# Kernel tuning notes

Measured on AMD Instinct MI355X. Metric: run time of the kernel, lower is better.

## Reference

```python
import jax, jax.numpy as jnp
import numpy as np

EPS = 1e-5
DEPTH = 4       # hash tree depth -> 16 buckets, 15 internal nodes
NBUCKETS = 16


def _bn_relu(x, g, b):
    # training-mode BatchNorm2d over (N,H,W) followed by ReLU
    m = x.mean((0, 2, 3), keepdims=True)
    v = x.var((0, 2, 3), keepdims=True)
    y = (x - m) * jax.lax.rsqrt(v + EPS)
    return jax.nn.relu(y * g[None, :, None, None] + b[None, :, None, None])


def _maddness_encode(sub, split_dims, thresholds):
    # sub: [R, Cb, L] subvectors; split_dims: [Cb, DEPTH] int; thresholds: [Cb, 15]
    R, Cb, _ = sub.shape
    carange = jnp.arange(Cb)[None, :]
    bucket = jnp.zeros((R, Cb), jnp.int32)
    for t in range(DEPTH):
        vals = jnp.take_along_axis(sub, split_dims[None, :, t][..., None], axis=2)[..., 0]  # [R,Cb]
        node = (2 ** t - 1) + bucket                     # node index at this tree level
        thr = thresholds[carange, node]                  # [R,Cb]
        bucket = 2 * bucket + (vals > thr).astype(jnp.int32)
    return bucket                                        # [R,Cb] in [0,16)


def _maddness_conv(x, split_dims, thresholds, lut, ksize, stride, pad):
    # hash-tree encode im2col patches per codebook, then LUT gather-and-sum
    N, C, H, W = x.shape
    patches = jax.lax.conv_general_dilated_patches(
        x, (ksize, ksize), (stride, stride), [(pad, pad), (pad, pad)])  # [N, C*k*k, Ho, Wo], channel-major
    _, Fdim, Ho, Wo = patches.shape
    Cb = split_dims.shape[0]
    sub = patches.transpose(0, 2, 3, 1).reshape(N * Ho * Wo, Cb, Fdim // Cb)
    codes = _maddness_encode(sub, split_dims, thresholds)
    onehot = jax.nn.one_hot(codes, NBUCKETS, dtype=lut.dtype)          # [R,Cb,16]
    out = jnp.einsum('rck,cko->ro', onehot, lut)                       # LUT gather-sum as GEMM
    return out.reshape(N, Ho, Wo, lut.shape[-1]).transpose(0, 3, 1, 2)


def setup_inputs() -> dict:
    key = jax.random.key(0)
    ks = jax.random.split(key, 16)
    P_in, P_out = 128, 256
    Cb1, Cb2, CbS = P_in, P_out, P_in // 4
    inp = {
        'x': jax.random.normal(ks[0], (32, P_in, 56, 56), jnp.float32),
        'bn1_g': jnp.ones((P_in,), jnp.float32),
        'bn1_b': jnp.zeros((P_in,), jnp.float32),
        'bn2_g': jnp.ones((P_out,), jnp.float32),
        'bn2_b': jnp.zeros((P_out,), jnp.float32),
        'thr1': jax.random.normal(ks[1], (Cb1, 15), jnp.float32),
        'lut1': 0.02 * jax.random.normal(ks[2], (Cb1, 16, P_out), jnp.float32),
        'thr2': jax.random.normal(ks[3], (Cb2, 15), jnp.float32),
        'lut2': 0.02 * jax.random.normal(ks[4], (Cb2, 16, P_out), jnp.float32),
        'thr_s': jax.random.normal(ks[5], (CbS, 15), jnp.float32),
        'lut_s': 0.02 * jax.random.normal(ks[6], (CbS, 16, P_out), jnp.float32),
        'fc1_w': 0.05 * jax.random.normal(ks[7], (P_out // 16, P_out), jnp.float32),
        'fc1_b': jnp.zeros((P_out // 16,), jnp.float32),
        'fc2_w': 0.05 * jax.random.normal(ks[8], (P_out, P_out // 16), jnp.float32),
        'fc2_b': jnp.zeros((P_out,), jnp.float32),
        'sd1': jax.random.randint(ks[9], (Cb1, DEPTH), 0, 9, jnp.int32),
        'sd2': jax.random.randint(ks[10], (Cb2, DEPTH), 0, 9, jnp.int32),
        'sd_s': jax.random.randint(ks[11], (CbS, DEPTH), 0, 4, jnp.int32),
    }
    return inp


def reference(x, bn1_g, bn1_b, bn2_g, bn2_b, thr1, lut1, thr2, lut2,
              thr_s, lut_s, fc1_w, fc1_b, fc2_w, fc2_b, sd1, sd2, sd_s):
    out = _bn_relu(x, bn1_g, bn1_b)
    shortcut = _maddness_conv(out, sd_s, thr_s, lut_s, 1, 2, 0)        # 1x1 stride-2 shortcut
    out = _maddness_conv(out, sd1, thr1, lut1, 3, 2, 1)                # conv1
    out = _maddness_conv(_bn_relu(out, bn2_g, bn2_b), sd2, thr2, lut2, 3, 1, 1)  # conv2
    # SE gate: global avg pool -> fc1 -> relu -> fc2 -> sigmoid
    w = out.mean((2, 3), keepdims=True)                                # [N,P,1,1]
    w = jax.nn.relu(jnp.einsum('nchw,oc->nohw', w, fc1_w) + fc1_b[None, :, None, None])
    w = jax.nn.sigmoid(jnp.einsum('nchw,oc->nohw', w, fc2_w) + fc2_b[None, :, None, None])
    return out * w + shortcut
```

## Files before the change

kernel.cpp:

```cpp
#include <hip/hip_runtime.h>
#include <hip/hip_bf16.h>
#include <math.h>

typedef unsigned char u8;
typedef unsigned int  u32;

#define N_    32
#define C1    128
#define H1    56
#define W1    56
#define HW1   (H1*W1)
#define CHW1  (C1*HW1)
#define C2    256
#define HO    28
#define WO    28
#define OHW   (HO*WO)
#define R_    (N_*OHW)

#define OFF_BN1S   ((size_t)0)
#define OFF_BN1Q   ((size_t)1024)
#define OFF_BN2S   ((size_t)2048)
#define OFF_BN2Q   ((size_t)4096)
#define OFF_POOL   ((size_t)6144)
#define OFF_SCALE1 ((size_t)38912)
#define OFF_SHIFT1 ((size_t)39936)
#define OFF_SCALE2 ((size_t)40960)
#define OFF_SHIFT2 ((size_t)43008)
#define OFF_GATE   ((size_t)45056)
#define OFF_CODE1  ((size_t)77824)
#define OFF_CODES  ((size_t)3289088)
#define OFF_CODE2  ((size_t)4091904)
#define OFF_OUT1   ((size_t)10514432)
#define OFF_SC     ((size_t)61894656)
#define OFF_OUT2   ((size_t)87584768)

__global__ __launch_bounds__(256) void k_bn1_stats(const float* __restrict__ x,
                                                   double* __restrict__ s1, double* __restrict__ q1) {
  __shared__ double rs[256], rq[256];
  int b = blockIdx.x; int c = b >> 3, chunk = b & 7;
  int tid = threadIdx.x;
  double s = 0.0, q = 0.0;
  for (int nn = chunk*4; nn < chunk*4 + 4; ++nn) {
    const float* p = x + (size_t)nn*CHW1 + (size_t)c*HW1;
    for (int i = tid; i < HW1; i += 256) { double v = (double)p[i]; s += v; q += v*v; }
  }
  rs[tid] = s; rq[tid] = q; __syncthreads();
  for (int st = 128; st > 0; st >>= 1) {
    if (tid < st) { rs[tid] += rs[tid+st]; rq[tid] += rq[tid+st]; }
    __syncthreads();
  }
  if (tid == 0) { atomicAdd(&s1[c], rs[0]); atomicAdd(&q1[c], rq[0]); }
}

__global__ __launch_bounds__(256) void k_fin(const double* __restrict__ s, const double* __restrict__ q,
                                             const float* __restrict__ g, const float* __restrict__ b,
                                             double* __restrict__ scale, double* __restrict__ shift,
                                             int nc, double cnt) {
  int c = blockIdx.x*blockDim.x + threadIdx.x;
  if (c >= nc) return;
  double m   = s[c] / cnt;
  double var = q[c] / cnt - m*m;
  double istd = 1.0 / sqrt(var + 1e-5);
  double sc = istd * (double)g[c];
  scale[c] = sc;
  shift[c] = (double)b[c] - m*sc;
}

__global__ __launch_bounds__(256) void k_enc1(const float* __restrict__ x,
                                              const int* __restrict__ sd1, const float* __restrict__ thr1,
                                              const int* __restrict__ sds, const float* __restrict__ thrs,
                                              const double* __restrict__ scale1, const double* __restrict__ shift1,
                                              u8* __restrict__ code1, u8* __restrict__ codes) {
  __shared__ double lsc[C1], lsh[C1];
  __shared__ float lthr[32*15];
  __shared__ u8 lsd[32][4];
  int tid = threadIdx.x;
  int y = blockIdx.y;
  int cbase = (y < 4) ? y*32 : 0;
  if (tid < C1) { lsc[tid] = scale1[tid]; lsh[tid] = shift1[tid]; }
  if (y < 4) {
    for (int i = tid; i < 32*15; i += 256) lthr[i] = thr1[cbase*15 + i];
    if (tid < 32) for (int j = 0; j < 4; ++j) lsd[tid][j] = (u8)sd1[(cbase+tid)*4 + j];
  } else {
    for (int i = tid; i < 32*15; i += 256) lthr[i] = thrs[i];
    if (tid < 32) for (int j = 0; j < 4; ++j) lsd[tid][j] = (u8)sds[tid*4 + j];
  }
  __syncthreads();
  int r = blockIdx.x*256 + tid;
  int n = r / OHW; int rem = r % OHW; int ho = rem / WO; int wo = rem % WO;
  const float* xn = x + (size_t)n*CHW1;
  if (y < 4) {
    for (int ci = 0; ci < 32; ++ci) {
      int c = cbase + ci;
      double sc = lsc[c], sh = lsh[c];
      int code = 0;
      #pragma unroll
      for (int t = 0; t < 4; ++t) {
        int sd = lsd[ci][t];
        int kh = sd / 3, kw = sd - kh*3;
        int ih = 2*ho + kh - 1, iw = 2*wo + kw - 1;
        double thr = (double)lthr[ci*15 + ((1<<t)-1) + code];
        int bit;
        if ((unsigned)ih < (unsigned)H1 && (unsigned)iw < (unsigned)W1) {
          double z = fma((double)xn[c*HW1 + ih*W1 + iw], sc, sh);
          z = z > 0.0 ? z : 0.0;
          bit = (z > thr) ? 1 : 0;
        } else {
          bit = (0.0 > thr) ? 1 : 0;
        }
        code = code + code + bit;
      }
      code1[(size_t)r*C1 + c] = (u8)code;
    }
  } else {
    int base = (2*ho)*W1 + 2*wo;
    for (int ci = 0; ci < 32; ++ci) {
      int code = 0;
      #pragma unroll
      for (int t = 0; t < 4; ++t) {
        int sd = lsd[ci][t];
        int ch = ci*4 + sd;
        double thr = (double)lthr[ci*15 + ((1<<t)-1) + code];
        double z = fma((double)xn[ch*HW1 + base], lsc[ch], lsh[ch]);
        z = z > 0.0 ? z : 0.0;
        int bit = (z > thr) ? 1 : 0;
        code = code + code + bit;
      }
      codes[(size_t)r*32 + ci] = (u8)code;
    }
  }
}

__global__ __launch_bounds__(256) void k_gather1(const u8* __restrict__ code1, const u8* __restrict__ codes,
                                                 const float* __restrict__ lut1, const float* __restrict__ luts,
                                                 double* __restrict__ out1, float* __restrict__ sc) {
  int l = threadIdx.x & 63;
  int r = blockIdx.x*4 + (threadIdx.x >> 6);
  const u32* cp = (const u32*)(code1 + (size_t)r*C1);
  const float4* L = (const float4*)lut1;
  double a0=0,a1=0,a2=0,a3=0;
  #pragma unroll 4
  for (int w = 0; w < 32; ++w) {
    u32 cv = cp[w];
    #pragma unroll
    for (int j = 0; j < 4; ++j) {
      int c = w*4 + j;
      int code = (cv >> (8*j)) & 15;
      float4 v = L[((c*16 + code) << 6) + l];
      a0 += (double)v.x; a1 += (double)v.y; a2 += (double)v.z; a3 += (double)v.w;
    }
  }
  float b0=0,b1=0,b2=0,b3=0;
  const u32* cps = (const u32*)(codes + (size_t)r*32);
  const float4* Ls = (const float4*)luts;
  #pragma unroll
  for (int w = 0; w < 8; ++w) {
    u32 cv = cps[w];
    #pragma unroll
    for (int j = 0; j < 4; ++j) {
      int c = w*4 + j;
      int code = (cv >> (8*j)) & 15;
      float4 v = Ls[((c*16 + code) << 6) + l];
      b0 += v.x; b1 += v.y; b2 += v.z; b3 += v.w;
    }
  }
  size_t o = (size_t)r*C2 + l*4;
  double2 d0; d0.x=a0; d0.y=a1;
  double2 d1; d1.x=a2; d1.y=a3;
  *(double2*)(out1 + o)     = d0;
  *(double2*)(out1 + o + 2) = d1;
  float4 bb; bb.x=b0; bb.y=b1; bb.z=b2; bb.w=b3;
  *(float4*)(sc + o) = bb;
}

__global__ __launch_bounds__(256) void k_bn2_stats(const double* __restrict__ out1,
                                                   double* __restrict__ s2, double* __restrict__ q2) {
  int o = threadIdx.x;
  int r0 = blockIdx.x * 128;
  double s = 0.0, q = 0.0;
  for (int j = 0; j < 128; ++j) {
    double v = out1[(size_t)(r0 + j)*C2 + o];
    s += v; q += v*v;
  }
  atomicAdd(&s2[o], s); atomicAdd(&q2[o], q);
}

__global__ __launch_bounds__(256) void k_enc2(const double* __restrict__ out1,
                                              const int* __restrict__ sd2, const float* __restrict__ thr2,
                                              const double* __restrict__ scale2, const double* __restrict__ shift2,
                                              u8* __restrict__ code2) {
  __shared__ float lthr[C2*15];
  __shared__ u8 lsd[C2][4];
  __shared__ double lsc[C2], lsh[C2];
  int tid = threadIdx.x;
  for (int i = tid; i < C2*15; i += 256) lthr[i] = thr2[i];
  for (int j = 0; j < 4; ++j) lsd[tid][j] = (u8)sd2[tid*4 + j];
  lsc[tid] = scale2[tid]; lsh[tid] = shift2[tid];
  __syncthreads();
  int c = tid;
  double scv = lsc[c], shv = lsh[c];
  int r0 = blockIdx.x*8;
  for (int rr = 0; rr < 8; ++rr) {
    int r = r0 + rr;
    int n = r / OHW; int rem = r % OHW; int ho = rem / WO; int wo = rem % WO;
    const double* on = out1 + (size_t)n*OHW*C2;
    int code = 0;
    #pragma unroll
    for (int t = 0; t < 4; ++t) {
      int sd = lsd[c][t];
      int kh = sd / 3, kw = sd - kh*3;
      int h = ho + kh - 1, w = wo + kw - 1;
      double thr = (double)lthr[c*15 + ((1<<t)-1) + code];
      int bit;
      if ((unsigned)h < (unsigned)HO && (unsigned)w < (unsigned)WO) {
        double z = fma(on[(size_t)(h*WO + w)*C2 + c], scv, shv);
        z = z > 0.0 ? z : 0.0;
        bit = (z > thr) ? 1 : 0;
      } else {
        bit = (0.0 > thr) ? 1 : 0;
      }
      code = code + code + bit;
    }
    code2[(size_t)r*C2 + c] = (u8)code;
  }
}

__global__ __launch_bounds__(256) void k_gather2(const u8* __restrict__ code2,
                                                 const float* __restrict__ lut2, float* __restrict__ out2) {
  int l = threadIdx.x & 63;
  int r = blockIdx.x*4 + (threadIdx.x >> 6);
  const u32* cp = (const u32*)(code2 + (size_t)r*C2);
  const float4* L = (const float4*)lut2;
  float a0=0,a1=0,a2=0,a3=0;
  #pragma unroll 4
  for (int w = 0; w < 64; ++w) {
    u32 cv = cp[w];
    #pragma unroll
    for (int j = 0; j < 4; ++j) {
      int c = w*4 + j;
      int code = (cv >> (8*j)) & 15;
      float4 v = L[((c*16 + code) << 6) + l];
      a0 += v.x; a1 += v.y; a2 += v.z; a3 += v.w;
    }
  }
  float4 res; res.x=a0; res.y=a1; res.z=a2; res.w=a3;
  *(float4*)(out2 + (size_t)r*C2 + l*4) = res;
}

__global__ __launch_bounds__(256) void k_pool(const float* __restrict__ out2, float* __restrict__ pool) {
  int n = blockIdx.x, seg = blockIdx.y, o = threadIdx.x;
  float s = 0.0f;
  int p0 = seg*112;
  for (int p = p0; p < p0 + 112; ++p) s += out2[(size_t)(n*OHW + p)*C2 + o];
  atomicAdd(&pool[n*C2 + o], s);
}

__global__ __launch_bounds__(256) void k_se(const float* __restrict__ pool,
                                            const float* __restrict__ w1, const float* __restrict__ b1f,
                                            const float* __restrict__ w2, const float* __restrict__ b2f,
                                            float* __restrict__ gate) {
  __shared__ float lp[C2];
  __shared__ float lh[16];
  int n = blockIdx.x, tid = threadIdx.x;
  lp[tid] = pool[n*C2 + tid] * (1.0f/(float)OHW);
  __syncthreads();
  if (tid < 16) {
    float s = b1f[tid];
    for (int c = 0; c < C2; ++c) s += lp[c]*w1[tid*C2 + c];
    lh[tid] = s > 0.0f ? s : 0.0f;
  }
  __syncthreads();
  float s = b2f[tid];
  #pragma unroll
  for (int i = 0; i < 16; ++i) s += lh[i]*w2[tid*16 + i];
  gate[n*C2 + tid] = 1.0f/(1.0f + expf(-s));
}

__global__ __launch_bounds__(256) void k_final(const float* __restrict__ out2, const float* __restrict__ scv,
                                               const float* __restrict__ gate, float* __restrict__ outp) {
  int idx = blockIdx.x*256 + threadIdx.x;
  int w = idx % WO; int t1 = idx / WO; int h = t1 % HO; int t2 = t1 / HO;
  int o = t2 & 255; int n = t2 >> 8;
  size_t rc = (size_t)(n*OHW + h*WO + w)*C2 + o;
  outp[idx] = out2[rc]*gate[n*C2 + o] + scv[rc];
}

extern "C" void kernel_launch(void* const* d_in, const int* in_sizes, int n_in,
                              void* d_out, int out_size, void* d_ws, size_t ws_size,
                              hipStream_t stream) {
  const float* x     = (const float*)d_in[0];
  const float* bn1_g = (const float*)d_in[1];
  const float* bn1_b = (const float*)d_in[2];
  const float* bn2_g = (const float*)d_in[3];
  const float* bn2_b = (const float*)d_in[4];
  const float* thr1  = (const float*)d_in[5];
  const float* lut1  = (const float*)d_in[6];
  const float* thr2  = (const float*)d_in[7];
  const float* lut2  = (const float*)d_in[8];
  const float* thr_s = (const float*)d_in[9];
  const float* lut_s = (const float*)d_in[10];
  const float* fc1_w = (const float*)d_in[11];
  const float* fc1_b = (const float*)d_in[12];
  const float* fc2_w = (const float*)d_in[13];
  const float* fc2_b = (const float*)d_in[14];
  const int*   sd1   = (const int*)d_in[15];
  const int*   sd2   = (const int*)d_in[16];
  const int*   sd_s  = (const int*)d_in[17];

  char* ws = (char*)d_ws;
  double* bn1s  = (double*)(ws + OFF_BN1S);
  double* bn1q  = (double*)(ws + OFF_BN1Q);
  double* bn2s  = (double*)(ws + OFF_BN2S);
  double* bn2q  = (double*)(ws + OFF_BN2Q);
  float*  pool  = (float*)(ws + OFF_POOL);
  double* scale1= (double*)(ws + OFF_SCALE1);
  double* shift1= (double*)(ws + OFF_SHIFT1);
  double* scale2= (double*)(ws + OFF_SCALE2);
  double* shift2= (double*)(ws + OFF_SHIFT2);
  float*  gate  = (float*)(ws + OFF_GATE);
  u8*     code1 = (u8*)(ws + OFF_CODE1);
  u8*     codes = (u8*)(ws + OFF_CODES);
  u8*     code2 = (u8*)(ws + OFF_CODE2);
  double* out1  = (double*)(ws + OFF_OUT1);
  float*  scb   = (float*)(ws + OFF_SC);
  float*  out2  = (float*)(ws + OFF_OUT2);
  float*  outp  = (float*)d_out;

  hipMemsetAsync(ws, 0, 38912, stream);

  k_bn1_stats<<<1024, 256, 0, stream>>>(x, bn1s, bn1q);
  k_fin<<<1, 128, 0, stream>>>(bn1s, bn1q, bn1_g, bn1_b, scale1, shift1, C1, (double)(N_*HW1));
  k_enc1<<<dim3(98, 5), 256, 0, stream>>>(x, sd1, thr1, sd_s, thr_s, scale1, shift1, code1, codes);
  k_gather1<<<R_/4, 256, 0, stream>>>(code1, codes, lut1, lut_s, out1, scb);
  k_bn2_stats<<<196, 256, 0, stream>>>(out1, bn2s, bn2q);
  k_fin<<<1, 256, 0, stream>>>(bn2s, bn2q, bn2_g, bn2_b, scale2, shift2, C2, (double)R_);
  k_enc2<<<R_/8, 256, 0, stream>>>(out1, sd2, thr2, scale2, shift2, code2);
  k_gather2<<<R_/4, 256, 0, stream>>>(code2, lut2, out2);
  k_pool<<<dim3(N_, 7), 256, 0, stream>>>(out2, pool);
  k_se<<<N_, 256, 0, stream>>>(pool, fc1_w, fc1_b, fc2_w, fc2_b, gate);
  k_final<<<(int)((size_t)N_*C2*OHW/256), 256, 0, stream>>>(out2, scb, gate, outp);
}
```

Measured before the change: 695.4 us.

## Pack codes to nibbles, use bf16 LUTs, fuse stats/pool, tile final transpose

```diff
diff --git a/kernel.cpp b/kernel.cpp
--- a/kernel.cpp
+++ b/kernel.cpp
@@ -4,6 +4,7 @@
 
 typedef unsigned char u8;
 typedef unsigned int  u32;
+typedef unsigned long long u64;
 
 #define N_    32
 #define C1    128
@@ -27,12 +28,30 @@
 #define OFF_SCALE2 ((size_t)40960)
 #define OFF_SHIFT2 ((size_t)43008)
 #define OFF_GATE   ((size_t)45056)
-#define OFF_CODE1  ((size_t)77824)
-#define OFF_CODES  ((size_t)3289088)
-#define OFF_CODE2  ((size_t)4091904)
-#define OFF_OUT1   ((size_t)10514432)
-#define OFF_SC     ((size_t)61894656)
-#define OFF_OUT2   ((size_t)87584768)
+#define OFF_C1P    ((size_t)77824)
+#define OFF_CS     ((size_t)1683456)
+#define OFF_LS16   ((size_t)2486272)
+#define OFF_L216   ((size_t)2748416)
+#define OFF_C2P    ((size_t)4845568)
+#define OFF_OUT1   ((size_t)8056832)
+#define OFF_SC     ((size_t)59437056)
+#define OFF_OUT2   ((size_t)85127168)
+
+__device__ inline float bf_lo(u32 p){ union{u32 u; float f;} t; t.u = p << 16;        return t.f; }
+__device__ inline float bf_hi(u32 p){ union{u32 u; float f;} t; t.u = p & 0xFFFF0000u; return t.f; }
+__device__ inline u32 rne_bf16(float f){ union{float f; u32 u;} t; t.f = f; return (t.u + 0x7FFFu + ((t.u >> 16) & 1u)) >> 16; }
+
+__global__ __launch_bounds__(256) void k_cvt(const float* __restrict__ lut2, const float* __restrict__ lut_s,
+                                             u32* __restrict__ d2, u32* __restrict__ ds_) {
+  int i = blockIdx.x*256 + threadIdx.x;
+  float4 v; uint2* dst; int base;
+  if (i < 262144) { v = ((const float4*)lut2)[i];          dst = (uint2*)d2;  base = i; }
+  else            { v = ((const float4*)lut_s)[i - 262144]; dst = (uint2*)ds_; base = i - 262144; }
+  uint2 o;
+  o.x = rne_bf16(v.x) | (rne_bf16(v.y) << 16);
+  o.y = rne_bf16(v.z) | (rne_bf16(v.w) << 16);
+  dst[base] = o;
+}
 
 __global__ __launch_bounds__(256) void k_bn1_stats(const float* __restrict__ x,
                                                    double* __restrict__ s1, double* __restrict__ q1) {
@@ -70,7 +89,7 @@
                                               const int* __restrict__ sd1, const float* __restrict__ thr1,
                                               const int* __restrict__ sds, const float* __restrict__ thrs,
                                               const double* __restrict__ scale1, const double* __restrict__ shift1,
-                                              u8* __restrict__ code1, u8* __restrict__ codes) {
+                                              u8* __restrict__ c1p, u8* __restrict__ codes) {
   __shared__ double lsc[C1], lsh[C1];
   __shared__ float lthr[32*15];
   __shared__ u8 lsd[32][4];
@@ -90,6 +109,7 @@
   int n = r / OHW; int rem = r % OHW; int ho = rem / WO; int wo = rem % WO;
   const float* xn = x + (size_t)n*CHW1;
   if (y < 4) {
+    u64 w0 = 0, w1 = 0;
     for (int ci = 0; ci < 32; ++ci) {
       int c = cbase + ci;
       double sc = lsc[c], sh = lsh[c];
@@ -110,8 +130,11 @@
         }
         code = code + code + bit;
       }
-      code1[(size_t)r*C1 + c] = (u8)code;
-    }
+      u64 cc = (u64)code << (4*(ci & 15));
+      if (ci < 16) w0 |= cc; else w1 |= cc;
+    }
+    ulonglong2 pk; pk.x = w0; pk.y = w1;
+    *(ulonglong2*)(c1p + (size_t)r*64 + (cbase >> 1)) = pk;
   } else {
     int base = (2*ho)*W1 + 2*wo;
     for (int ci = 0; ci < 32; ++ci) {
@@ -131,28 +154,31 @@
   }
 }
 
-__global__ __launch_bounds__(256) void k_gather1(const u8* __restrict__ code1, const u8* __restrict__ codes,
-                                                 const float* __restrict__ lut1, const float* __restrict__ luts,
-                                                 double* __restrict__ out1, float* __restrict__ sc) {
-  int l = threadIdx.x & 63;
-  int r = blockIdx.x*4 + (threadIdx.x >> 6);
-  const u32* cp = (const u32*)(code1 + (size_t)r*C1);
+__global__ __launch_bounds__(256) void k_gather1(const u8* __restrict__ c1p, const u8* __restrict__ codes,
+                                                 const float* __restrict__ lut1, const uint2* __restrict__ lutS16,
+                                                 double* __restrict__ out1, float* __restrict__ sc,
+                                                 double* __restrict__ s2, double* __restrict__ q2) {
+  __shared__ double red[4][256];
+  int tid = threadIdx.x;
+  int l = tid & 63;
+  int wid = tid >> 6;
+  int r = blockIdx.x*4 + wid;
+  const u32* cp = (const u32*)(c1p + (size_t)r*64);
   const float4* L = (const float4*)lut1;
   double a0=0,a1=0,a2=0,a3=0;
-  #pragma unroll 4
-  for (int w = 0; w < 32; ++w) {
+  #pragma unroll 2
+  for (int w = 0; w < 16; ++w) {
     u32 cv = cp[w];
     #pragma unroll
-    for (int j = 0; j < 4; ++j) {
-      int c = w*4 + j;
-      int code = (cv >> (8*j)) & 15;
+    for (int j = 0; j < 8; ++j) {
+      int c = w*8 + j;
+      int code = (cv >> (4*j)) & 15;
       float4 v = L[((c*16 + code) << 6) + l];
       a0 += (double)v.x; a1 += (double)v.y; a2 += (double)v.z; a3 += (double)v.w;
     }
   }
   float b0=0,b1=0,b2=0,b3=0;
   const u32* cps = (const u32*)(codes + (size_t)r*32);
-  const float4* Ls = (const float4*)luts;
   #pragma unroll
   for (int w = 0; w < 8; ++w) {
     u32 cv = cps[w];
@@ -160,8 +186,8 @@
     for (int j = 0; j < 4; ++j) {
       int c = w*4 + j;
       int code = (cv >> (8*j)) & 15;
-      float4 v = Ls[((c*16 + code) << 6) + l];
-      b0 += v.x; b1 += v.y; b2 += v.z; b3 += v.w;
+      uint2 v = lutS16[((c*16 + code) << 6) + l];
+      b0 += bf_lo(v.x); b1 += bf_hi(v.x); b2 += bf_lo(v.y); b3 += bf_hi(v.y);
     }
   }
   size_t o = (size_t)r*C2 + l*4;
@@ -171,24 +197,21 @@
   *(double2*)(out1 + o + 2) = d1;
   float4 bb; bb.x=b0; bb.y=b1; bb.z=b2; bb.w=b3;
   *(float4*)(sc + o) = bb;
-}
-
-__global__ __launch_bounds__(256) void k_bn2_stats(const double* __restrict__ out1,
-                                                   double* __restrict__ s2, double* __restrict__ q2) {
-  int o = threadIdx.x;
-  int r0 = blockIdx.x * 128;
-  double s = 0.0, q = 0.0;
-  for (int j = 0; j < 128; ++j) {
-    double v = out1[(size_t)(r0 + j)*C2 + o];
-    s += v; q += v*v;
-  }
-  atomicAdd(&s2[o], s); atomicAdd(&q2[o], q);
+  red[wid][l*4+0]=a0; red[wid][l*4+1]=a1; red[wid][l*4+2]=a2; red[wid][l*4+3]=a3;
+  __syncthreads();
+  double s = red[0][tid] + red[1][tid] + red[2][tid] + red[3][tid];
+  atomicAdd(&s2[tid], s);
+  __syncthreads();
+  red[wid][l*4+0]=a0*a0; red[wid][l*4+1]=a1*a1; red[wid][l*4+2]=a2*a2; red[wid][l*4+3]=a3*a3;
+  __syncthreads();
+  double q = red[0][tid] + red[1][tid] + red[2][tid] + red[3][tid];
+  atomicAdd(&q2[tid], q);
 }
 
 __global__ __launch_bounds__(256) void k_enc2(const double* __restrict__ out1,
                                               const int* __restrict__ sd2, const float* __restrict__ thr2,
                                               const double* __restrict__ scale2, const double* __restrict__ shift2,
-                                              u8* __restrict__ code2) {
+                                              u8* __restrict__ c2p) {
   __shared__ float lthr[C2*15];
   __shared__ u8 lsd[C2][4];
   __shared__ double lsc[C2], lsh[C2];
@@ -221,38 +244,39 @@
       }
       code = code + code + bit;
     }
-    code2[(size_t)r*C2 + c] = (u8)code;
-  }
-}
-
-__global__ __launch_bounds__(256) void k_gather2(const u8* __restrict__ code2,
-                                                 const float* __restrict__ lut2, float* __restrict__ out2) {
-  int l = threadIdx.x & 63;
-  int r = blockIdx.x*4 + (threadIdx.x >> 6);
-  const u32* cp = (const u32*)(code2 + (size_t)r*C2);
-  const float4* L = (const float4*)lut2;
+    int partner = __shfl_xor(code, 1);
+    if (!(tid & 1)) c2p[(size_t)r*128 + (c >> 1)] = (u8)(code | (partner << 4));
+  }
+}
+
+__global__ __launch_bounds__(256) void k_gather2(const u8* __restrict__ c2p,
+                                                 const uint2* __restrict__ lut216,
+                                                 float* __restrict__ out2, float* __restrict__ pool) {
+  __shared__ float red[4][256];
+  int tid = threadIdx.x;
+  int l = tid & 63;
+  int wid = tid >> 6;
+  int r = blockIdx.x*4 + wid;
+  const u32* cp = (const u32*)(c2p + (size_t)r*128);
   float a0=0,a1=0,a2=0,a3=0;
-  #pragma unroll 4
-  for (int w = 0; w < 64; ++w) {
+  #pragma unroll 2
+  for (int w = 0; w < 32; ++w) {
     u32 cv = cp[w];
     #pragma unroll
-    for (int j = 0; j < 4; ++j) {
-      int c = w*4 + j;
-      int code = (cv >> (8*j)) & 15;
-      float4 v = L[((c*16 + code) << 6) + l];
-      a0 += v.x; a1 += v.y; a2 += v.z; a3 += v.w;
+    for (int j = 0; j < 8; ++j) {
+      int c = w*8 + j;
+      int code = (cv >> (4*j)) & 15;
+      uint2 v = lut216[((c*16 + code) << 6) + l];
+      a0 += bf_lo(v.x); a1 += bf_hi(v.x); a2 += bf_lo(v.y); a3 += bf_hi(v.y);
     }
   }
   float4 res; res.x=a0; res.y=a1; res.z=a2; res.w=a3;
   *(float4*)(out2 + (size_t)r*C2 + l*4) = res;
-}
-
-__global__ __launch_bounds__(256) void k_pool(const float* __restrict__ out2, float* __restrict__ pool) {
-  int n = blockIdx.x, seg = blockIdx.y, o = threadIdx.x;
-  float s = 0.0f;
-  int p0 = seg*112;
-  for (int p = p0; p < p0 + 112; ++p) s += out2[(size_t)(n*OHW + p)*C2 + o];
-  atomicAdd(&pool[n*C2 + o], s);
+  int n = blockIdx.x / 196;
+  red[wid][l*4+0]=a0; red[wid][l*4+1]=a1; red[wid][l*4+2]=a2; red[wid][l*4+3]=a3;
+  __syncthreads();
+  float p = red[0][tid] + red[1][tid] + red[2][tid] + red[3][tid];
+  atomicAdd(&pool[n*C2 + tid], p);
 }
 
 __global__ __launch_bounds__(256) void k_se(const float* __restrict__ pool,
@@ -278,11 +302,24 @@
 
 __global__ __launch_bounds__(256) void k_final(const float* __restrict__ out2, const float* __restrict__ scv,
                                                const float* __restrict__ gate, float* __restrict__ outp) {
-  int idx = blockIdx.x*256 + threadIdx.x;
-  int w = idx % WO; int t1 = idx / WO; int h = t1 % HO; int t2 = t1 / HO;
-  int o = t2 & 255; int n = t2 >> 8;
-  size_t rc = (size_t)(n*OHW + h*WO + w)*C2 + o;
-  outp[idx] = out2[rc]*gate[n*C2 + o] + scv[rc];
+  __shared__ float tile[64][113];
+  int n = blockIdx.x, chb = blockIdx.y, pxb = blockIdx.z;
+  int l = threadIdx.x & 63, w4 = threadIdx.x >> 6;
+  float g = gate[n*C2 + chb*64 + l];
+  int pxbase = pxb*112;
+  #pragma unroll 4
+  for (int i = 0; i < 28; ++i) {
+    int px = i*4 + w4;
+    size_t rc = ((size_t)(n*OHW + pxbase + px))*C2 + chb*64 + l;
+    tile[l][px] = out2[rc]*g + scv[rc];
+  }
+  __syncthreads();
+  #pragma unroll 4
+  for (int j = 0; j < 28; ++j) {
+    int flat = j*256 + threadIdx.x;
+    int ch = flat / 112, px = flat - ch*112;
+    outp[((size_t)(n*C2 + chb*64 + ch))*OHW + pxbase + px] = tile[ch][px];
+  }
 }
 
 extern "C" void kernel_launch(void* const* d_in, const int* in_sizes, int n_in,
@@ -318,9 +355,11 @@
   double* scale2= (double*)(ws + OFF_SCALE2);
   double* shift2= (double*)(ws + OFF_SHIFT2);
   float*  gate  = (float*)(ws + OFF_GATE);
-  u8*     code1 = (u8*)(ws + OFF_CODE1);
-  u8*     codes = (u8*)(ws + OFF_CODES);
-  u8*     code2 = (u8*)(ws + OFF_CODE2);
+  u8*     c1p   = (u8*)(ws + OFF_C1P);
+  u8*     codes = (u8*)(ws + OFF_CS);
+  u32*    ls16  = (u32*)(ws + OFF_LS16);
+  u32*    l216  = (u32*)(ws + OFF_L216);
+  u8*     c2p   = (u8*)(ws + OFF_C2P);
   double* out1  = (double*)(ws + OFF_OUT1);
   float*  scb   = (float*)(ws + OFF_SC);
   float*  out2  = (float*)(ws + OFF_OUT2);
@@ -328,15 +367,14 @@
 
   hipMemsetAsync(ws, 0, 38912, stream);
 
+  k_cvt<<<1152, 256, 0, stream>>>(lut2, lut_s, l216, ls16);
   k_bn1_stats<<<1024, 256, 0, stream>>>(x, bn1s, bn1q);
   k_fin<<<1, 128, 0, stream>>>(bn1s, bn1q, bn1_g, bn1_b, scale1, shift1, C1, (double)(N_*HW1));
-  k_enc1<<<dim3(98, 5), 256, 0, stream>>>(x, sd1, thr1, sd_s, thr_s, scale1, shift1, code1, codes);
-  k_gather1<<<R_/4, 256, 0, stream>>>(code1, codes, lut1, lut_s, out1, scb);
-  k_bn2_stats<<<196, 256, 0, stream>>>(out1, bn2s, bn2q);
+  k_enc1<<<dim3(98, 5), 256, 0, stream>>>(x, sd1, thr1, sd_s, thr_s, scale1, shift1, c1p, codes);
+  k_gather1<<<R_/4, 256, 0, stream>>>(c1p, codes, lut1, (const uint2*)ls16, out1, scb, bn2s, bn2q);
   k_fin<<<1, 256, 0, stream>>>(bn2s, bn2q, bn2_g, bn2_b, scale2, shift2, C2, (double)R_);
-  k_enc2<<<R_/8, 256, 0, stream>>>(out1, sd2, thr2, scale2, shift2, code2);
-  k_gather2<<<R_/4, 256, 0, stream>>>(code2, lut2, out2);
-  k_pool<<<dim3(N_, 7), 256, 0, stream>>>(out2, pool);
+  k_enc2<<<R_/8, 256, 0, stream>>>(out1, sd2, thr2, scale2, shift2, c2p);
+  k_gather2<<<R_/4, 256, 0, stream>>>(c2p, (const uint2*)l216, out2, pool);
   k_se<<<N_, 256, 0, stream>>>(pool, fc1_w, fc1_b, fc2_w, fc2_b, gate);
-  k_final<<<(int)((size_t)N_*C2*OHW/256), 256, 0, stream>>>(out2, scb, gate, outp);
-}
+  k_final<<<dim3(N_, 4, 7), 256, 0, stream>>>(out2, scb, gate, outp);
+}
```

New measurement: 643.8 us. 1.08x faster.
